# Performance work log

Hardware: AMD Instinct MI355X
Metric: run time of the kernel (lower is better)

Reference implementation:

```python
import jax, jax.numpy as jnp
import numpy as np

H = 16        # num_attention_heads
KV = 4        # num_key_value_heads
HD = 128      # head_dim = hidden_size // H
ROPE_THETA = 10000.0


def _rotate_half(x):
    x1, x2 = jnp.split(x, 2, axis=-1)
    return jnp.concatenate([-x2, x1], axis=-1)


def _rope_cos_sin(seq_len, dtype):
    # inv_freq: (HD//2,), full rotary (partial_rotary_factor=1.0), attention_scaling=1.0
    inv_freq = 1.0 / (ROPE_THETA ** (jnp.arange(0, HD, 2, dtype=jnp.float32) / HD))
    pos = jnp.arange(seq_len, dtype=jnp.float32)
    freqs = pos[:, None] * inv_freq[None, :]              # (S, HD//2)
    emb = jnp.concatenate([freqs, freqs], axis=-1)        # (S, HD)
    # expansion_axis=2 -> broadcast over heads: (1, S, 1, HD)
    return (jnp.cos(emb)[None, :, None, :].astype(dtype),
            jnp.sin(emb)[None, :, None, :].astype(dtype))


def setup_inputs() -> dict:
    key = jax.random.key(0)
    k1, k2, k3, k4, k5 = jax.random.split(key, 5)
    B, S, D = 2, 2048, 2048
    hidden_states = jax.random.normal(k1, (B, S, D), dtype=jnp.float32)
    # causal mask, True = attend
    causal = jnp.tril(jnp.ones((S, S), dtype=bool))
    attention_mask = jnp.broadcast_to(causal[None, None, :, :], (B, 1, S, S))
    scale = 0.02
    Wq = jax.random.normal(k2, (D, H * HD), dtype=jnp.float32) * scale
    Wk = jax.random.normal(k3, (D, KV * HD), dtype=jnp.float32) * scale
    Wv = jax.random.normal(k4, (D, KV * HD), dtype=jnp.float32) * scale
    Wo = jax.random.normal(k5, (H, HD, D), dtype=jnp.float32) * scale
    return {"hidden_states": hidden_states, "attention_mask": attention_mask,
            "Wq": Wq, "Wk": Wk, "Wv": Wv, "Wo": Wo}


def reference(hidden_states, attention_mask, Wq, Wk, Wv, Wo):
    B, S, D = hidden_states.shape
    q = (hidden_states @ Wq).reshape(B, S, H, HD)   # bquh
    k = (hidden_states @ Wk).reshape(B, S, KV, HD)
    v = (hidden_states @ Wv).reshape(B, S, KV, HD)

    cos, sin = _rope_cos_sin(S, q.dtype)
    q = q * cos + _rotate_half(q) * sin
    k = k * cos + _rotate_half(k) * sin

    # GQA: repeat kv heads to match query heads
    groups = H // KV
    k = jnp.repeat(k, groups, axis=2)               # (B, S, H, HD)
    v = jnp.repeat(v, groups, axis=2)

    inv_norm = 1.0 / np.sqrt(HD)
    scores = jnp.einsum('bquh,bkuh->buqk', q, k) * inv_norm   # (B, H, Sq, Sk)
    scores = scores.astype(jnp.float32)
    neg = jnp.asarray(-1e9, dtype=jnp.float32)
    scores = jnp.where(attention_mask, scores, neg)
    probs = jax.nn.softmax(scores, axis=-1).astype(q.dtype)
    attn = jnp.einsum('buqk,bkuh->bquh', probs, v)             # (B, S, H, HD)
    out = jnp.einsum('bquh,uhm->bqm', attn, Wo)                # (B, S, D)
    return out
```

## Files before the change

### kernel.cpp

```cpp
#include <hip/hip_runtime.h>
#include <math.h>

namespace {

constexpr int B   = 2;
constexpr int S   = 2048;
constexpr int D   = 2048;
constexpr int NH  = 16;
constexpr int NKV = 4;
constexpr int HD  = 128;
constexpr int GRP = NH / NKV;

typedef __attribute__((ext_vector_type(8))) short  short8;
typedef __attribute__((ext_vector_type(4))) float  f32x4;
typedef unsigned short u16;

__device__ inline u16 f2bf(float f) {
    unsigned u = __float_as_uint(f);
    u = (u + 0x7FFFu + ((u >> 16) & 1u)) >> 16;
    return (u16)u;
}
__device__ inline float bf2f(u16 h) {
    return __uint_as_float((unsigned)h << 16);
}

__device__ __forceinline__ void gload_lds16(const void* g, void* l) {
    __builtin_amdgcn_global_load_lds(
        (const __attribute__((address_space(1))) unsigned int*)g,
        (__attribute__((address_space(3))) unsigned int*)l, 16, 0, 0);
}

__global__ __launch_bounds__(256)
void split_cast_kernel(const float* __restrict__ X, u16* __restrict__ H,
                       u16* __restrict__ L, int n4)
{
    const int idx = blockIdx.x * 256 + threadIdx.x;
    if (idx >= n4) return;
    const float4 v = reinterpret_cast<const float4*>(X)[idx];
    ushort4 h, l;
    h.x = f2bf(v.x); l.x = f2bf(v.x - bf2f(h.x));
    h.y = f2bf(v.y); l.y = f2bf(v.y - bf2f(h.y));
    h.z = f2bf(v.z); l.z = f2bf(v.z - bf2f(h.z));
    h.w = f2bf(v.w); l.w = f2bf(v.w - bf2f(h.w));
    reinterpret_cast<ushort4*>(H)[idx] = h;
    reinterpret_cast<ushort4*>(L)[idx] = l;
}

__global__ __launch_bounds__(256)
void wcast_t_kernel(const float* __restrict__ W, u16* __restrict__ Th,
                    u16* __restrict__ Tl, int Nw, int n_off)
{
    __shared__ u16 th[64][68];
    __shared__ u16 tl[64][68];
    const int t  = threadIdx.x;
    const int n0 = blockIdx.x * 64;
    const int k0 = blockIdx.y * 64;

#pragma unroll
    for (int i = 0; i < 4; ++i) {
        const int kr = (t >> 4) + i * 16;
        const int nc = (t & 15) * 4;
        const float4 v = *reinterpret_cast<const float4*>(
            &W[(size_t)(k0 + kr) * Nw + n0 + nc]);
        const u16 hx = f2bf(v.x), hy = f2bf(v.y), hz = f2bf(v.z), hw = f2bf(v.w);
        th[kr][nc + 0] = hx; tl[kr][nc + 0] = f2bf(v.x - bf2f(hx));
        th[kr][nc + 1] = hy; tl[kr][nc + 1] = f2bf(v.y - bf2f(hy));
        th[kr][nc + 2] = hz; tl[kr][nc + 2] = f2bf(v.z - bf2f(hz));
        th[kr][nc + 3] = hw; tl[kr][nc + 3] = f2bf(v.w - bf2f(hw));
    }
    __syncthreads();
#pragma unroll
    for (int i = 0; i < 4; ++i) {
        const int nr = (t >> 4) + i * 16;
        const int kc = (t & 15) * 4;
        ushort4 oh, ol;
        oh.x = th[kc + 0][nr]; ol.x = tl[kc + 0][nr];
        oh.y = th[kc + 1][nr]; ol.y = tl[kc + 1][nr];
        oh.z = th[kc + 2][nr]; ol.z = tl[kc + 2][nr];
        oh.w = th[kc + 3][nr]; ol.w = tl[kc + 3][nr];
        const size_t o = (size_t)(n_off + n0 + nr) * 2048 + k0 + kc;
        *reinterpret_cast<ushort4*>(&Th[o]) = oh;
        *reinterpret_cast<ushort4*>(&Tl[o]) = ol;
    }
}

__global__ __launch_bounds__(256)
void hgemm_hilo_kernel(const u16* __restrict__ Ah, const u16* __restrict__ Al,
                       const u16* __restrict__ Bth, const u16* __restrict__ Btl,
                       float* __restrict__ C, int M, int N, int K)
{
    __shared__ alignas(16) u16 AsH[4096];
    __shared__ alignas(16) u16 AsL[4096];
    __shared__ alignas(16) u16 BsH[4096];
    __shared__ alignas(16) u16 BsL[4096];

    const int t  = threadIdx.x;
    const int w  = t >> 6;
    const int l  = t & 63;
    const int lc = l & 15;
    const int kg = l >> 4;
    const int wr = w >> 1, wc = w & 1;

    const int m0 = blockIdx.y * 128;
    const int n0 = blockIdx.x * 128;

    const int srow = l >> 2;
    const int sblk = l & 3;

    f32x4 acc[4][4];
#pragma unroll
    for (int i = 0; i < 4; ++i)
#pragma unroll
        for (int j = 0; j < 4; ++j) acc[i][j] = (f32x4){0.f, 0.f, 0.f, 0.f};

    for (int k0 = 0; k0 < K; k0 += 32) {
#pragma unroll
        for (int i = 0; i < 2; ++i) {
            const int c   = i * 4 + w;
            const int row = c * 16 + srow;
            const int swb = sblk ^ ((row >> 1) & 3);
            const size_t ga = (size_t)(m0 + row) * K + k0 + swb * 8;
            const size_t gb = (size_t)(n0 + row) * K + k0 + swb * 8;
            u16* ldst = (u16*)nullptr;
            (void)ldst;
            gload_lds16(Ah  + ga, AsH + c * 512);
            gload_lds16(Al  + ga, AsL + c * 512);
            gload_lds16(Bth + gb, BsH + c * 512);
            gload_lds16(Btl + gb, BsL + c * 512);
        }
        __syncthreads();

        short8 fah[4], fal[4], fbh[4], fbl[4];
#pragma unroll
        for (int i = 0; i < 4; ++i) {
            const int ra = wr * 64 + i * 16 + lc;
            const int oa = ra * 32 + ((kg ^ ((ra >> 1) & 3)) * 8);
            fah[i] = *reinterpret_cast<const short8*>(&AsH[oa]);
            fal[i] = *reinterpret_cast<const short8*>(&AsL[oa]);
            const int rb = wc * 64 + i * 16 + lc;
            const int ob = rb * 32 + ((kg ^ ((rb >> 1) & 3)) * 8);
            fbh[i] = *reinterpret_cast<const short8*>(&BsH[ob]);
            fbl[i] = *reinterpret_cast<const short8*>(&BsL[ob]);
        }
#pragma unroll
        for (int i = 0; i < 4; ++i)
#pragma unroll
            for (int j = 0; j < 4; ++j) {
                acc[i][j] = __builtin_amdgcn_mfma_f32_16x16x32_bf16(
                    fal[i], fbh[j], acc[i][j], 0, 0, 0);
                acc[i][j] = __builtin_amdgcn_mfma_f32_16x16x32_bf16(
                    fah[i], fbl[j], acc[i][j], 0, 0, 0);
                acc[i][j] = __builtin_amdgcn_mfma_f32_16x16x32_bf16(
                    fah[i], fbh[j], acc[i][j], 0, 0, 0);
            }
        __syncthreads();
    }

#pragma unroll
    for (int i = 0; i < 4; ++i)
#pragma unroll
        for (int j = 0; j < 4; ++j)
#pragma unroll
            for (int r = 0; r < 4; ++r) {
                const int m = m0 + wr * 64 + i * 16 + kg * 4 + r;
                const int n = n0 + wc * 64 + j * 16 + lc;
                C[(size_t)m * N + n] = acc[i][j][r];
            }
}

__global__ __launch_bounds__(256)
void rope_cast_kernel(const float* __restrict__ X, int stride, int col_off,
                      u16* __restrict__ Yh, u16* __restrict__ Yl,
                      int n_heads, int total_pairs, float scale)
{
    const int idx = blockIdx.x * 256 + threadIdx.x;
    if (idx >= total_pairs) return;
    const int i    = idx & 63;
    const int rest = idx >> 6;
    const int head = rest % n_heads;
    const int row  = rest / n_heads;
    const int s    = row & (S - 1);
    const int b    = row >> 11;

    const float inv = expf(-9.2103403719761836f * (float)i * (1.0f / 64.0f));
    float sn, cs;
    sincosf((float)s * inv, &sn, &cs);

    const float* src = X + (size_t)row * stride + col_off + head * HD + i;
    const float x1 = src[0], x2 = src[64];
    const float y1 = (x1 * cs - x2 * sn) * scale;
    const float y2 = (x2 * cs + x1 * sn) * scale;

    const u16 h1 = f2bf(y1), h2 = f2bf(y2);
    const size_t o = ((size_t)(b * n_heads + head) * S + s) * HD + i;
    Yh[o] = h1;  Yh[o + 64] = h2;
    Yl[o]      = f2bf(y1 - bf2f(h1));
    Yl[o + 64] = f2bf(y2 - bf2f(h2));
}

__global__ __launch_bounds__(256)
void vcast_kernel(const float* __restrict__ V, int stride, int col_off,
                  u16* __restrict__ Yh, u16* __restrict__ Yl)
{
    __shared__ u16 th[64][68];
    __shared__ u16 tl[64][68];
    const int t  = threadIdx.x;
    const int s0 = blockIdx.x * 64, dv0 = blockIdx.y * 64;
    const int b  = blockIdx.z >> 2, u = blockIdx.z & 3;

#pragma unroll
    for (int i = 0; i < 4; ++i) {
        const int sr = (t >> 4) + i * 16;
        const int dc = (t & 15) * 4;
        const float4 v = *reinterpret_cast<const float4*>(
            &V[(size_t)(b * S + s0 + sr) * stride + col_off + u * HD + dv0 + dc]);
        const u16 hx = f2bf(v.x), hy = f2bf(v.y), hz = f2bf(v.z), hw = f2bf(v.w);
        th[sr][dc + 0] = hx; tl[sr][dc + 0] = f2bf(v.x - bf2f(hx));
        th[sr][dc + 1] = hy; tl[sr][dc + 1] = f2bf(v.y - bf2f(hy));
        th[sr][dc + 2] = hz; tl[sr][dc + 2] = f2bf(v.z - bf2f(hz));
        th[sr][dc + 3] = hw; tl[sr][dc + 3] = f2bf(v.w - bf2f(hw));
    }
    __syncthreads();
#pragma unroll
    for (int i = 0; i < 4; ++i) {
        const int dr = (t >> 4) + i * 16;
        const int sc = (t & 15) * 4;
        ushort4 oh, ol;
        oh.x = th[sc + 0][dr]; ol.x = tl[sc + 0][dr];
        oh.y = th[sc + 1][dr]; ol.y = tl[sc + 1][dr];
        oh.z = th[sc + 2][dr]; ol.z = tl[sc + 2][dr];
        oh.w = th[sc + 3][dr]; ol.w = tl[sc + 3][dr];
        const size_t o = ((size_t)(b * NKV + u) * HD + dv0 + dr) * S + s0 + sc;
        *reinterpret_cast<ushort4*>(&Yh[o]) = oh;
        *reinterpret_cast<ushort4*>(&Yl[o]) = ol;
    }
}

constexpr int QTILE = 64, KT = 32;

__global__ __launch_bounds__(256)
void flash_mfma_kernel(const u16* __restrict__ Qh, const u16* __restrict__ Ql,
                       const u16* __restrict__ Kh, const u16* __restrict__ Kl,
                       const u16* __restrict__ Vh, const u16* __restrict__ Vl,
                       u16* __restrict__ Oh, u16* __restrict__ Ol)
{
    __shared__ alignas(16) u16 smem[23552];
    u16* KsH = smem;
    u16* KsL = smem + 4096;
    u16* VtH = smem + 8192;
    u16* VtL = smem + 13312;
    u16* PH  = smem + 18432;
    u16* PL  = smem + 20992;

    const int t  = threadIdx.x;
    const int w  = t >> 6;
    const int ln = t & 63;
    const int lg = ln >> 4;
    const int lc = ln & 15;

    const int qt = (int)gridDim.x - 1 - (int)blockIdx.x;
    const int q0 = qt * QTILE;
    const int bh = blockIdx.y;
    const int b  = bh / NH, h = bh % NH, u = h / GRP;

    const size_t qbase = (size_t)(b * NH + h) * S * HD;
    const size_t kbase = (size_t)(b * NKV + u) * S * HD;
    const size_t vbase = (size_t)(b * NKV + u) * HD * S;

    {
        u16* QsH = smem;
        u16* QsL = smem + 8192;
#pragma unroll
        for (int i = 0; i < 4; ++i) {
            const int r = (t >> 4) + i * 16;
            const int blk = t & 15;
            const size_t src = qbase + (size_t)(q0 + r) * HD + blk * 8;
            const int dst = r * 128 + ((blk ^ (r & 7)) * 8);
            *reinterpret_cast<short8*>(&QsH[dst]) =
                *reinterpret_cast<const short8*>(&Qh[src]);
            *reinterpret_cast<short8*>(&QsL[dst]) =
                *reinterpret_cast<const short8*>(&Ql[src]);
        }
        __syncthreads();
    }
    short8 qah[4], qal[4];
#pragma unroll
    for (int ks = 0; ks < 4; ++ks) {
        const int qr = w * 16 + lc;
        const int off = qr * 128 + (((ks * 4 + lg) ^ (qr & 7)) * 8);
        qah[ks] = *reinterpret_cast<const short8*>(&smem[off]);
        qal[ks] = *reinterpret_cast<const short8*>(&smem[8192 + off]);
    }
    __syncthreads();

    f32x4 o[8];
#pragma unroll
    for (int i = 0; i < 8; ++i) o[i] = (f32x4){0.f, 0.f, 0.f, 0.f};
    float m_run[4] = {-1e30f, -1e30f, -1e30f, -1e30f};
    float l_run[4] = {0.f, 0.f, 0.f, 0.f};

    u16* PwH = PH + w * 640;
    u16* PwL = PL + w * 640;
    const int qw0 = q0 + w * 16;
    const int nkt = q0 / KT + 2;

    for (int kt = 0; kt < nkt; ++kt) {
        const int k0 = kt * KT;
#pragma unroll
        for (int i = 0; i < 2; ++i) {
            const int r = (t >> 4) + i * 16;
            const int blk = t & 15;
            const size_t src = kbase + (size_t)(k0 + r) * HD + blk * 8;
            const int dst = r * 128 + ((blk ^ (r & 7)) * 8);
            *reinterpret_cast<short8*>(&KsH[dst]) =
                *reinterpret_cast<const short8*>(&Kh[src]);
            *reinterpret_cast<short8*>(&KsL[dst]) =
                *reinterpret_cast<const short8*>(&Kl[src]);
        }
#pragma unroll
        for (int i = 0; i < 2; ++i) {
            const int dv = (t >> 2) + i * 64;
            const int blk = t & 3;
            const size_t src = vbase + (size_t)dv * S + k0 + blk * 8;
            const int dst = dv * 40 + blk * 8;
            *reinterpret_cast<short8*>(&VtH[dst]) =
                *reinterpret_cast<const short8*>(&Vh[src]);
            *reinterpret_cast<short8*>(&VtL[dst]) =
                *reinterpret_cast<const short8*>(&Vl[src]);
        }
        __syncthreads();

        f32x4 a0 = {0.f, 0.f, 0.f, 0.f}, a1 = {0.f, 0.f, 0.f, 0.f};
#pragma unroll
        for (int ks = 0; ks < 4; ++ks) {
            const int r0 = lc, r1 = 16 + lc;
            const int o0b = r0 * 128 + (((ks * 4 + lg) ^ (r0 & 7)) * 8);
            const int o1b = r1 * 128 + (((ks * 4 + lg) ^ (r1 & 7)) * 8);
            const short8 kb0h = *reinterpret_cast<const short8*>(&KsH[o0b]);
            const short8 kb0l = *reinterpret_cast<const short8*>(&KsL[o0b]);
            const short8 kb1h = *reinterpret_cast<const short8*>(&KsH[o1b]);
            const short8 kb1l = *reinterpret_cast<const short8*>(&KsL[o1b]);
            a0 = __builtin_amdgcn_mfma_f32_16x16x32_bf16(qal[ks], kb0h, a0, 0, 0, 0);
            a0 = __builtin_amdgcn_mfma_f32_16x16x32_bf16(qah[ks], kb0l, a0, 0, 0, 0);
            a0 = __builtin_amdgcn_mfma_f32_16x16x32_bf16(qah[ks], kb0h, a0, 0, 0, 0);
            a1 = __builtin_amdgcn_mfma_f32_16x16x32_bf16(qal[ks], kb1h, a1, 0, 0, 0);
            a1 = __builtin_amdgcn_mfma_f32_16x16x32_bf16(qah[ks], kb1l, a1, 0, 0, 0);
            a1 = __builtin_amdgcn_mfma_f32_16x16x32_bf16(qah[ks], kb1h, a1, 0, 0, 0);
        }

        const bool need_mask = (k0 + KT - 1 > qw0);
#pragma unroll
        for (int r = 0; r < 4; ++r) {
            float s0 = a0[r], s1 = a1[r];
            const int qg = qw0 + lg * 4 + r;
            if (need_mask) {
                if (k0 + lc > qg)      s0 = -1e30f;
                if (k0 + 16 + lc > qg) s1 = -1e30f;
            }
            float mx = fmaxf(s0, s1);
            mx = fmaxf(mx, __shfl_xor(mx, 1, 64));
            mx = fmaxf(mx, __shfl_xor(mx, 2, 64));
            mx = fmaxf(mx, __shfl_xor(mx, 4, 64));
            mx = fmaxf(mx, __shfl_xor(mx, 8, 64));
            const float mn  = fmaxf(m_run[r], mx);
            const float rsc = __expf(m_run[r] - mn);
            const float p0  = __expf(s0 - mn);
            const float p1  = __expf(s1 - mn);
            float rs = p0 + p1;
            rs += __shfl_xor(rs, 1, 64);
            rs += __shfl_xor(rs, 2, 64);
            rs += __shfl_xor(rs, 4, 64);
            rs += __shfl_xor(rs, 8, 64);
            l_run[r] = l_run[r] * rsc + rs;
            m_run[r] = mn;
#pragma unroll
            for (int nt = 0; nt < 8; ++nt) o[nt][r] *= rsc;
            const u16 p0h = f2bf(p0);
            const u16 p1h = f2bf(p1);
            const int row = (lg * 4 + r) * 40;
            PwH[row + lc]      = p0h;
            PwH[row + 16 + lc] = p1h;
            PwL[row + lc]      = f2bf(p0 - bf2f(p0h));
            PwL[row + 16 + lc] = f2bf(p1 - bf2f(p1h));
        }
        asm volatile("s_waitcnt lgkmcnt(0)" ::: "memory");

        const short8 pah = *reinterpret_cast<const short8*>(&PwH[lc * 40 + lg * 8]);
        const short8 pal = *reinterpret_cast<const short8*>(&PwL[lc * 40 + lg * 8]);
#pragma unroll
        for (int nt = 0; nt < 8; ++nt) {
            const int dvo = (nt * 16 + lc) * 40 + lg * 8;
            const short8 vbh = *reinterpret_cast<const short8*>(&VtH[dvo]);
            const short8 vbl = *reinterpret_cast<const short8*>(&VtL[dvo]);
            o[nt] = __builtin_amdgcn_mfma_f32_16x16x32_bf16(pal, vbh, o[nt], 0, 0, 0);
            o[nt] = __builtin_amdgcn_mfma_f32_16x16x32_bf16(pah, vbl, o[nt], 0, 0, 0);
            o[nt] = __builtin_amdgcn_mfma_f32_16x16x32_bf16(pah, vbh, o[nt], 0, 0, 0);
        }
        __syncthreads();
    }

    float invl[4];
#pragma unroll
    for (int r = 0; r < 4; ++r) invl[r] = 1.f / l_run[r];
#pragma unroll
    for (int nt = 0; nt < 8; ++nt) {
#pragma unroll
        for (int r = 0; r < 4; ++r) {
            const float v = o[nt][r] * invl[r];
            const size_t off =
                (size_t)(b * S + qw0 + lg * 4 + r) * (NH * HD) + h * HD + nt * 16 + lc;
            const u16 hv = f2bf(v);
            Oh[off] = hv;
            Ol[off] = f2bf(v - bf2f(hv));
        }
    }
}

}

extern "C" void kernel_launch(void* const* d_in, const int* in_sizes, int n_in,
                              void* d_out, int out_size, void* d_ws, size_t ws_size,
                              hipStream_t stream)
{
    const float* hidden = (const float*)d_in[0];
    const float* Wq = (const float*)d_in[2];
    const float* Wk = (const float*)d_in[3];
    const float* Wv = (const float*)d_in[4];
    const float* Wo = (const float*)d_in[5];
    float* out = (float*)d_out;

    char* wsb = (char*)d_ws;
    u16*   hid_hi  = (u16*)(wsb);
    u16*   hid_lo  = (u16*)(wsb + 16777216);
    float* qkv_f   = (float*)(wsb + 33554432);
    u16*   k_hi    = (u16*)(wsb + 83886080);
    u16*   k_lo    = (u16*)(wsb + 88080384);
    u16*   v_hi    = (u16*)(wsb + 92274688);
    u16*   v_lo    = (u16*)(wsb + 96468992);
    u16*   wT_hi   = (u16*)(wsb + 100663296);
    u16*   wT_lo   = (u16*)(wsb + 113246208);
    u16* q_hi    = hid_hi;
    u16* q_lo    = hid_lo;
    u16* attn_hi = (u16*)(wsb + 33554432);
    u16* attn_lo = (u16*)(wsb + 50331648);
    u16* woT_hi  = wT_hi;
    u16* woT_lo  = wT_lo;

    const dim3 blk(256);

    split_cast_kernel<<<dim3(8192), blk, 0, stream>>>(hidden, hid_hi, hid_lo, 2097152);
    wcast_t_kernel<<<dim3(32, 32), blk, 0, stream>>>(Wq, wT_hi, wT_lo, 2048, 0);
    wcast_t_kernel<<<dim3(8, 32),  blk, 0, stream>>>(Wk, wT_hi, wT_lo, 512, 2048);
    wcast_t_kernel<<<dim3(8, 32),  blk, 0, stream>>>(Wv, wT_hi, wT_lo, 512, 2560);
    hgemm_hilo_kernel<<<dim3(24, 32), blk, 0, stream>>>(
        hid_hi, hid_lo, wT_hi, wT_lo, qkv_f, 4096, 3072, 2048);
    wcast_t_kernel<<<dim3(32, 32), blk, 0, stream>>>(Wo, woT_hi, woT_lo, 2048, 0);
    const int qpairs = 4096 * NH * 64;
    const int kpairs = 4096 * NKV * 64;
    rope_cast_kernel<<<dim3(qpairs / 256), blk, 0, stream>>>(
        qkv_f, 3072, 0, q_hi, q_lo, NH, qpairs, 0.08838834764831845f);
    rope_cast_kernel<<<dim3(kpairs / 256), blk, 0, stream>>>(
        qkv_f, 3072, 2048, k_hi, k_lo, NKV, kpairs, 1.0f);
    vcast_kernel<<<dim3(32, 2, 8), blk, 0, stream>>>(
        qkv_f, 3072, 2560, v_hi, v_lo);
    flash_mfma_kernel<<<dim3(S / QTILE, B * NH), blk, 0, stream>>>(
        q_hi, q_lo, k_hi, k_lo, v_hi, v_lo, attn_hi, attn_lo);
    hgemm_hilo_kernel<<<dim3(16, 32), blk, 0, stream>>>(
        attn_hi, attn_lo, woT_hi, woT_lo, out, 4096, 2048, 2048);
}
```

Before: 807.3 us.

## Load Q/K/V fragments directly from global, drop LDS staging and block syncs

The flash attention kernel now reads Q, K and V MFMA fragments straight from global memory into registers instead of staging them cooperatively in shared memory. Removing the staging also drops the per-tile __syncthreads, so each wave iterates independently and stops at its own causal limit (qw0/KT+1) instead of the block-wide limit. The MFMA blocks are wrapped in s_setprio to favour matrix issue. The cost is that the four waves, and sibling heads in a GQA group, now each fetch the same K/V data separately, which raises global and L2 traffic and register pressure.

```diff
diff --git a/kernel.cpp b/kernel.cpp
--- a/kernel.cpp
+++ b/kernel.cpp
@@ -121,8 +121,6 @@
             const int swb = sblk ^ ((row >> 1) & 3);
             const size_t ga = (size_t)(m0 + row) * K + k0 + swb * 8;
             const size_t gb = (size_t)(n0 + row) * K + k0 + swb * 8;
-            u16* ldst = (u16*)nullptr;
-            (void)ldst;
             gload_lds16(Ah  + ga, AsH + c * 512);
             gload_lds16(Al  + ga, AsL + c * 512);
             gload_lds16(Bth + gb, BsH + c * 512);
@@ -244,13 +242,8 @@
                        const u16* __restrict__ Vh, const u16* __restrict__ Vl,
                        u16* __restrict__ Oh, u16* __restrict__ Ol)
 {
-    __shared__ alignas(16) u16 smem[23552];
-    u16* KsH = smem;
-    u16* KsL = smem + 4096;
-    u16* VtH = smem + 8192;
-    u16* VtL = smem + 13312;
-    u16* PH  = smem + 18432;
-    u16* PL  = smem + 20992;
+    __shared__ alignas(16) u16 PHs[4 * 640];
+    __shared__ alignas(16) u16 PLs[4 * 640];
 
     const int t  = threadIdx.x;
     const int w  = t >> 6;
@@ -267,31 +260,17 @@
     const size_t kbase = (size_t)(b * NKV + u) * S * HD;
     const size_t vbase = (size_t)(b * NKV + u) * HD * S;
 
+    const int qw0 = q0 + w * 16;
+
+    short8 qah[4], qal[4];
     {
-        u16* QsH = smem;
-        u16* QsL = smem + 8192;
-#pragma unroll
-        for (int i = 0; i < 4; ++i) {
-            const int r = (t >> 4) + i * 16;
-            const int blk = t & 15;
-            const size_t src = qbase + (size_t)(q0 + r) * HD + blk * 8;
-            const int dst = r * 128 + ((blk ^ (r & 7)) * 8);
-            *reinterpret_cast<short8*>(&QsH[dst]) =
-                *reinterpret_cast<const short8*>(&Qh[src]);
-            *reinterpret_cast<short8*>(&QsL[dst]) =
-                *reinterpret_cast<const short8*>(&Ql[src]);
-        }
-        __syncthreads();
-    }
-    short8 qah[4], qal[4];
-#pragma unroll
-    for (int ks = 0; ks < 4; ++ks) {
-        const int qr = w * 16 + lc;
-        const int off = qr * 128 + (((ks * 4 + lg) ^ (qr & 7)) * 8);
-        qah[ks] = *reinterpret_cast<const short8*>(&smem[off]);
-        qal[ks] = *reinterpret_cast<const short8*>(&smem[8192 + off]);
-    }
-    __syncthreads();
+        const size_t qr = qbase + (size_t)(qw0 + lc) * HD + lg * 8;
+#pragma unroll
+        for (int ks = 0; ks < 4; ++ks) {
+            qah[ks] = *reinterpret_cast<const short8*>(&Qh[qr + ks * 32]);
+            qal[ks] = *reinterpret_cast<const short8*>(&Ql[qr + ks * 32]);
+        }
+    }
 
     f32x4 o[8];
 #pragma unroll
@@ -299,53 +278,46 @@
     float m_run[4] = {-1e30f, -1e30f, -1e30f, -1e30f};
     float l_run[4] = {0.f, 0.f, 0.f, 0.f};
 
-    u16* PwH = PH + w * 640;
-    u16* PwL = PL + w * 640;
-    const int qw0 = q0 + w * 16;
-    const int nkt = q0 / KT + 2;
+    u16* PwH = PHs + w * 640;
+    u16* PwL = PLs + w * 640;
+
+    const int nkt = qw0 / KT + 1;
 
     for (int kt = 0; kt < nkt; ++kt) {
         const int k0 = kt * KT;
-#pragma unroll
-        for (int i = 0; i < 2; ++i) {
-            const int r = (t >> 4) + i * 16;
-            const int blk = t & 15;
-            const size_t src = kbase + (size_t)(k0 + r) * HD + blk * 8;
-            const int dst = r * 128 + ((blk ^ (r & 7)) * 8);
-            *reinterpret_cast<short8*>(&KsH[dst]) =
-                *reinterpret_cast<const short8*>(&Kh[src]);
-            *reinterpret_cast<short8*>(&KsL[dst]) =
-                *reinterpret_cast<const short8*>(&Kl[src]);
-        }
-#pragma unroll
-        for (int i = 0; i < 2; ++i) {
-            const int dv = (t >> 2) + i * 64;
-            const int blk = t & 3;
-            const size_t src = vbase + (size_t)dv * S + k0 + blk * 8;
-            const int dst = dv * 40 + blk * 8;
-            *reinterpret_cast<short8*>(&VtH[dst]) =
-                *reinterpret_cast<const short8*>(&Vh[src]);
-            *reinterpret_cast<short8*>(&VtL[dst]) =
-                *reinterpret_cast<const short8*>(&Vl[src]);
-        }
-        __syncthreads();
+
+        short8 kb0h[4], kb0l[4], kb1h[4], kb1l[4];
+        {
+            const size_t kr0 = kbase + (size_t)(k0 + lc) * HD + lg * 8;
+            const size_t kr1 = kr0 + (size_t)16 * HD;
+#pragma unroll
+            for (int ks = 0; ks < 4; ++ks) {
+                kb0h[ks] = *reinterpret_cast<const short8*>(&Kh[kr0 + ks * 32]);
+                kb0l[ks] = *reinterpret_cast<const short8*>(&Kl[kr0 + ks * 32]);
+                kb1h[ks] = *reinterpret_cast<const short8*>(&Kh[kr1 + ks * 32]);
+                kb1l[ks] = *reinterpret_cast<const short8*>(&Kl[kr1 + ks * 32]);
+            }
+        }
 
         f32x4 a0 = {0.f, 0.f, 0.f, 0.f}, a1 = {0.f, 0.f, 0.f, 0.f};
+        __builtin_amdgcn_s_setprio(1);
 #pragma unroll
         for (int ks = 0; ks < 4; ++ks) {
-            const int r0 = lc, r1 = 16 + lc;
-            const int o0b = r0 * 128 + (((ks * 4 + lg) ^ (r0 & 7)) * 8);
-            const int o1b = r1 * 128 + (((ks * 4 + lg) ^ (r1 & 7)) * 8);
-            const short8 kb0h = *reinterpret_cast<const short8*>(&KsH[o0b]);
-            const short8 kb0l = *reinterpret_cast<const short8*>(&KsL[o0b]);
-            const short8 kb1h = *reinterpret_cast<const short8*>(&KsH[o1b]);
-            const short8 kb1l = *reinterpret_cast<const short8*>(&KsL[o1b]);
-            a0 = __builtin_amdgcn_mfma_f32_16x16x32_bf16(qal[ks], kb0h, a0, 0, 0, 0);
-            a0 = __builtin_amdgcn_mfma_f32_16x16x32_bf16(qah[ks], kb0l, a0, 0, 0, 0);
-            a0 = __builtin_amdgcn_mfma_f32_16x16x32_bf16(qah[ks], kb0h, a0, 0, 0, 0);
-            a1 = __builtin_amdgcn_mfma_f32_16x16x32_bf16(qal[ks], kb1h, a1, 0, 0, 0);
-            a1 = __builtin_amdgcn_mfma_f32_16x16x32_bf16(qah[ks], kb1l, a1, 0, 0, 0);
-            a1 = __builtin_amdgcn_mfma_f32_16x16x32_bf16(qah[ks], kb1h, a1, 0, 0, 0);
+            a0 = __builtin_amdgcn_mfma_f32_16x16x32_bf16(qal[ks], kb0h[ks], a0, 0, 0, 0);
+            a0 = __builtin_amdgcn_mfma_f32_16x16x32_bf16(qah[ks], kb0l[ks], a0, 0, 0, 0);
+            a0 = __builtin_amdgcn_mfma_f32_16x16x32_bf16(qah[ks], kb0h[ks], a0, 0, 0, 0);
+            a1 = __builtin_amdgcn_mfma_f32_16x16x32_bf16(qal[ks], kb1h[ks], a1, 0, 0, 0);
+            a1 = __builtin_amdgcn_mfma_f32_16x16x32_bf16(qah[ks], kb1l[ks], a1, 0, 0, 0);
+            a1 = __builtin_amdgcn_mfma_f32_16x16x32_bf16(qah[ks], kb1h[ks], a1, 0, 0, 0);
+        }
+        __builtin_amdgcn_s_setprio(0);
+
+        short8 vbh[8], vbl[8];
+#pragma unroll
+        for (int nt = 0; nt < 8; ++nt) {
+            const size_t vo = vbase + (size_t)(nt * 16 + lc) * S + k0 + lg * 8;
+            vbh[nt] = *reinterpret_cast<const short8*>(&Vh[vo]);
+            vbl[nt] = *reinterpret_cast<const short8*>(&Vl[vo]);
         }
 
         const bool need_mask = (k0 + KT - 1 > qw0);
@@ -387,16 +359,14 @@
 
         const short8 pah = *reinterpret_cast<const short8*>(&PwH[lc * 40 + lg * 8]);
         const short8 pal = *reinterpret_cast<const short8*>(&PwL[lc * 40 + lg * 8]);
+        __builtin_amdgcn_s_setprio(1);
 #pragma unroll
         for (int nt = 0; nt < 8; ++nt) {
-            const int dvo = (nt * 16 + lc) * 40 + lg * 8;
-            const short8 vbh = *reinterpret_cast<const short8*>(&VtH[dvo]);
-            const short8 vbl = *reinterpret_cast<const short8*>(&VtL[dvo]);
-            o[nt] = __builtin_amdgcn_mfma_f32_16x16x32_bf16(pal, vbh, o[nt], 0, 0, 0);
-            o[nt] = __builtin_amdgcn_mfma_f32_16x16x32_bf16(pah, vbl, o[nt], 0, 0, 0);
-            o[nt] = __builtin_amdgcn_mfma_f32_16x16x32_bf16(pah, vbh, o[nt], 0, 0, 0);
-        }
-        __syncthreads();
+            o[nt] = __builtin_amdgcn_mfma_f32_16x16x32_bf16(pal, vbh[nt], o[nt], 0, 0, 0);
+            o[nt] = __builtin_amdgcn_mfma_f32_16x16x32_bf16(pah, vbl[nt], o[nt], 0, 0, 0);
+            o[nt] = __builtin_amdgcn_mfma_f32_16x16x32_bf16(pah, vbh[nt], o[nt], 0, 0, 0);
+        }
+        __builtin_amdgcn_s_setprio(0);
     }
 
     float invl[4];
```

Result: slower. 1.329 ms (+64.7%).

## Prefetch next K/V tile into registers and add lazy softmax rescaling in attention

Applied to the files above, without the earlier changes.

The attention loop now loads the next K/V tile from global memory into registers while computing on the current tile in LDS, overlapping global latency with the MFMA work. Warps whose 16 query rows lie entirely above the current key tile skip that tile's compute. The online softmax rescales the output only when a row max grows by more than 8, checked wave-wide, and the per-row reductions are batched so shuffles interleave. s_setprio is raised around the MFMA blocks. The register staging adds VGPR pressure, which can reduce occupancy, and the lazy max leaves exponentials bounded by e^8 rather than 1.

```diff
diff --git a/kernel.cpp b/kernel.cpp
--- a/kernel.cpp
+++ b/kernel.cpp
@@ -121,8 +121,6 @@
             const int swb = sblk ^ ((row >> 1) & 3);
             const size_t ga = (size_t)(m0 + row) * K + k0 + swb * 8;
             const size_t gb = (size_t)(n0 + row) * K + k0 + swb * 8;
-            u16* ldst = (u16*)nullptr;
-            (void)ldst;
             gload_lds16(Ah  + ga, AsH + c * 512);
             gload_lds16(Al  + ga, AsL + c * 512);
             gload_lds16(Bth + gb, BsH + c * 512);
@@ -304,100 +302,150 @@
     const int qw0 = q0 + w * 16;
     const int nkt = q0 / KT + 2;
 
+    const int sr_k = t >> 4;
+    const int sb_k = t & 15;
+    const int sr_v = t >> 2;
+    const int sb_v = t & 3;
+    const int dKsw = (sb_k ^ (sr_k & 7)) * 8;
+    const int dK0  = sr_k * 128 + dKsw;
+    const int dK1  = (sr_k + 16) * 128 + dKsw;
+    const int dV0  = sr_v * 40 + sb_v * 8;
+    const int dV1  = (sr_v + 64) * 40 + sb_v * 8;
+
+    short8 stg[8];
+#define LOADTILE(K0)                                                          \
+    {                                                                         \
+        const size_t ksrc = kbase + (size_t)((K0) + sr_k) * HD + sb_k * 8;    \
+        stg[0] = *reinterpret_cast<const short8*>(&Kh[ksrc]);                 \
+        stg[1] = *reinterpret_cast<const short8*>(&Kh[ksrc + 16 * HD]);       \
+        stg[2] = *reinterpret_cast<const short8*>(&Kl[ksrc]);                 \
+        stg[3] = *reinterpret_cast<const short8*>(&Kl[ksrc + 16 * HD]);       \
+        const size_t vsrc = vbase + (size_t)sr_v * S + (K0) + sb_v * 8;       \
+        stg[4] = *reinterpret_cast<const short8*>(&Vh[vsrc]);                 \
+        stg[5] = *reinterpret_cast<const short8*>(&Vh[vsrc + (size_t)64 * S]);\
+        stg[6] = *reinterpret_cast<const short8*>(&Vl[vsrc]);                 \
+        stg[7] = *reinterpret_cast<const short8*>(&Vl[vsrc + (size_t)64 * S]);\
+    }
+
+    LOADTILE(0);
+
     for (int kt = 0; kt < nkt; ++kt) {
         const int k0 = kt * KT;
-#pragma unroll
-        for (int i = 0; i < 2; ++i) {
-            const int r = (t >> 4) + i * 16;
-            const int blk = t & 15;
-            const size_t src = kbase + (size_t)(k0 + r) * HD + blk * 8;
-            const int dst = r * 128 + ((blk ^ (r & 7)) * 8);
-            *reinterpret_cast<short8*>(&KsH[dst]) =
-                *reinterpret_cast<const short8*>(&Kh[src]);
-            *reinterpret_cast<short8*>(&KsL[dst]) =
-                *reinterpret_cast<const short8*>(&Kl[src]);
-        }
-#pragma unroll
-        for (int i = 0; i < 2; ++i) {
-            const int dv = (t >> 2) + i * 64;
-            const int blk = t & 3;
-            const size_t src = vbase + (size_t)dv * S + k0 + blk * 8;
-            const int dst = dv * 40 + blk * 8;
-            *reinterpret_cast<short8*>(&VtH[dst]) =
-                *reinterpret_cast<const short8*>(&Vh[src]);
-            *reinterpret_cast<short8*>(&VtL[dst]) =
-                *reinterpret_cast<const short8*>(&Vl[src]);
+        *reinterpret_cast<short8*>(&KsH[dK0]) = stg[0];
+        *reinterpret_cast<short8*>(&KsH[dK1]) = stg[1];
+        *reinterpret_cast<short8*>(&KsL[dK0]) = stg[2];
+        *reinterpret_cast<short8*>(&KsL[dK1]) = stg[3];
+        *reinterpret_cast<short8*>(&VtH[dV0]) = stg[4];
+        *reinterpret_cast<short8*>(&VtH[dV1]) = stg[5];
+        *reinterpret_cast<short8*>(&VtL[dV0]) = stg[6];
+        *reinterpret_cast<short8*>(&VtL[dV1]) = stg[7];
+        __syncthreads();
+
+        if (kt + 1 < nkt) LOADTILE(k0 + KT);
+
+        if (k0 <= qw0 + 15) {
+            f32x4 a0 = {0.f, 0.f, 0.f, 0.f}, a1 = {0.f, 0.f, 0.f, 0.f};
+            __builtin_amdgcn_s_setprio(1);
+#pragma unroll
+            for (int ks = 0; ks < 4; ++ks) {
+                const int r0 = lc, r1 = 16 + lc;
+                const int o0b = r0 * 128 + (((ks * 4 + lg) ^ (r0 & 7)) * 8);
+                const int o1b = r1 * 128 + (((ks * 4 + lg) ^ (r1 & 7)) * 8);
+                const short8 kb0h = *reinterpret_cast<const short8*>(&KsH[o0b]);
+                const short8 kb0l = *reinterpret_cast<const short8*>(&KsL[o0b]);
+                const short8 kb1h = *reinterpret_cast<const short8*>(&KsH[o1b]);
+                const short8 kb1l = *reinterpret_cast<const short8*>(&KsL[o1b]);
+                a0 = __builtin_amdgcn_mfma_f32_16x16x32_bf16(qal[ks], kb0h, a0, 0, 0, 0);
+                a0 = __builtin_amdgcn_mfma_f32_16x16x32_bf16(qah[ks], kb0l, a0, 0, 0, 0);
+                a0 = __builtin_amdgcn_mfma_f32_16x16x32_bf16(qah[ks], kb0h, a0, 0, 0, 0);
+                a1 = __builtin_amdgcn_mfma_f32_16x16x32_bf16(qal[ks], kb1h, a1, 0, 0, 0);
+                a1 = __builtin_amdgcn_mfma_f32_16x16x32_bf16(qah[ks], kb1l, a1, 0, 0, 0);
+                a1 = __builtin_amdgcn_mfma_f32_16x16x32_bf16(qah[ks], kb1h, a1, 0, 0, 0);
+            }
+            __builtin_amdgcn_s_setprio(0);
+
+            float s0v[4], s1v[4], mx[4];
+            const bool need_mask = (k0 + KT - 1 > qw0);
+#pragma unroll
+            for (int r = 0; r < 4; ++r) {
+                float s0 = a0[r], s1 = a1[r];
+                const int qg = qw0 + lg * 4 + r;
+                if (need_mask) {
+                    if (k0 + lc > qg)      s0 = -1e30f;
+                    if (k0 + 16 + lc > qg) s1 = -1e30f;
+                }
+                s0v[r] = s0; s1v[r] = s1;
+                mx[r] = fmaxf(s0, s1);
+            }
+#pragma unroll
+            for (int off = 1; off < 16; off <<= 1)
+#pragma unroll
+                for (int r = 0; r < 4; ++r)
+                    mx[r] = fmaxf(mx[r], __shfl_xor(mx[r], off, 64));
+
+            bool grow = false;
+#pragma unroll
+            for (int r = 0; r < 4; ++r) grow = grow || (mx[r] > m_run[r] + 8.0f);
+            const bool resc_needed = __any((int)grow);
+
+            float mn[4], rsc[4];
+#pragma unroll
+            for (int r = 0; r < 4; ++r) {
+                mn[r]  = resc_needed ? fmaxf(m_run[r], mx[r]) : m_run[r];
+                rsc[r] = resc_needed ? __expf(m_run[r] - mn[r]) : 1.0f;
+            }
+            float p0[4], p1[4], rs[4];
+#pragma unroll
+            for (int r = 0; r < 4; ++r) {
+                p0[r] = __expf(s0v[r] - mn[r]);
+                p1[r] = __expf(s1v[r] - mn[r]);
+                rs[r] = p0[r] + p1[r];
+            }
+#pragma unroll
+            for (int off = 1; off < 16; off <<= 1)
+#pragma unroll
+                for (int r = 0; r < 4; ++r)
+                    rs[r] += __shfl_xor(rs[r], off, 64);
+#pragma unroll
+            for (int r = 0; r < 4; ++r) {
+                l_run[r] = l_run[r] * rsc[r] + rs[r];
+                m_run[r] = mn[r];
+            }
+            if (resc_needed) {
+#pragma unroll
+                for (int nt = 0; nt < 8; ++nt)
+#pragma unroll
+                    for (int r = 0; r < 4; ++r) o[nt][r] *= rsc[r];
+            }
+#pragma unroll
+            for (int r = 0; r < 4; ++r) {
+                const u16 p0h = f2bf(p0[r]);
+                const u16 p1h = f2bf(p1[r]);
+                const int row = (lg * 4 + r) * 40;
+                PwH[row + lc]      = p0h;
+                PwH[row + 16 + lc] = p1h;
+                PwL[row + lc]      = f2bf(p0[r] - bf2f(p0h));
+                PwL[row + 16 + lc] = f2bf(p1[r] - bf2f(p1h));
+            }
+            asm volatile("s_waitcnt lgkmcnt(0)" ::: "memory");
+
+            const short8 pah = *reinterpret_cast<const short8*>(&PwH[lc * 40 + lg * 8]);
+            const short8 pal = *reinterpret_cast<const short8*>(&PwL[lc * 40 + lg * 8]);
+            __builtin_amdgcn_s_setprio(1);
+#pragma unroll
+            for (int nt = 0; nt < 8; ++nt) {
+                const int dvo = (nt * 16 + lc) * 40 + lg * 8;
+                const short8 vbh = *reinterpret_cast<const short8*>(&VtH[dvo]);
+                const short8 vbl = *reinterpret_cast<const short8*>(&VtL[dvo]);
+                o[nt] = __builtin_amdgcn_mfma_f32_16x16x32_bf16(pal, vbh, o[nt], 0, 0, 0);
+                o[nt] = __builtin_amdgcn_mfma_f32_16x16x32_bf16(pah, vbl, o[nt], 0, 0, 0);
+                o[nt] = __builtin_amdgcn_mfma_f32_16x16x32_bf16(pah, vbh, o[nt], 0, 0, 0);
+            }
+            __builtin_amdgcn_s_setprio(0);
         }
         __syncthreads();
-
-        f32x4 a0 = {0.f, 0.f, 0.f, 0.f}, a1 = {0.f, 0.f, 0.f, 0.f};
-#pragma unroll
-        for (int ks = 0; ks < 4; ++ks) {
-            const int r0 = lc, r1 = 16 + lc;
-            const int o0b = r0 * 128 + (((ks * 4 + lg) ^ (r0 & 7)) * 8);
-            const int o1b = r1 * 128 + (((ks * 4 + lg) ^ (r1 & 7)) * 8);
-            const short8 kb0h = *reinterpret_cast<const short8*>(&KsH[o0b]);
-            const short8 kb0l = *reinterpret_cast<const short8*>(&KsL[o0b]);
-            const short8 kb1h = *reinterpret_cast<const short8*>(&KsH[o1b]);
-            const short8 kb1l = *reinterpret_cast<const short8*>(&KsL[o1b]);
-            a0 = __builtin_amdgcn_mfma_f32_16x16x32_bf16(qal[ks], kb0h, a0, 0, 0, 0);
-            a0 = __builtin_amdgcn_mfma_f32_16x16x32_bf16(qah[ks], kb0l, a0, 0, 0, 0);
-            a0 = __builtin_amdgcn_mfma_f32_16x16x32_bf16(qah[ks], kb0h, a0, 0, 0, 0);
-            a1 = __builtin_amdgcn_mfma_f32_16x16x32_bf16(qal[ks], kb1h, a1, 0, 0, 0);
-            a1 = __builtin_amdgcn_mfma_f32_16x16x32_bf16(qah[ks], kb1l, a1, 0, 0, 0);
-            a1 = __builtin_amdgcn_mfma_f32_16x16x32_bf16(qah[ks], kb1h, a1, 0, 0, 0);
-        }
-
-        const bool need_mask = (k0 + KT - 1 > qw0);
-#pragma unroll
-        for (int r = 0; r < 4; ++r) {
-            float s0 = a0[r], s1 = a1[r];
-            const int qg = qw0 + lg * 4 + r;
-            if (need_mask) {
-                if (k0 + lc > qg)      s0 = -1e30f;
-                if (k0 + 16 + lc > qg) s1 = -1e30f;
-            }
-            float mx = fmaxf(s0, s1);
-            mx = fmaxf(mx, __shfl_xor(mx, 1, 64));
-            mx = fmaxf(mx, __shfl_xor(mx, 2, 64));
-            mx = fmaxf(mx, __shfl_xor(mx, 4, 64));
-            mx = fmaxf(mx, __shfl_xor(mx, 8, 64));
-            const float mn  = fmaxf(m_run[r], mx);
-            const float rsc = __expf(m_run[r] - mn);
-            const float p0  = __expf(s0 - mn);
-            const float p1  = __expf(s1 - mn);
-            float rs = p0 + p1;
-            rs += __shfl_xor(rs, 1, 64);
-            rs += __shfl_xor(rs, 2, 64);
-            rs += __shfl_xor(rs, 4, 64);
-            rs += __shfl_xor(rs, 8, 64);
-            l_run[r] = l_run[r] * rsc + rs;
-            m_run[r] = mn;
-#pragma unroll
-            for (int nt = 0; nt < 8; ++nt) o[nt][r] *= rsc;
-            const u16 p0h = f2bf(p0);
-            const u16 p1h = f2bf(p1);
-            const int row = (lg * 4 + r) * 40;
-            PwH[row + lc]      = p0h;
-            PwH[row + 16 + lc] = p1h;
-            PwL[row + lc]      = f2bf(p0 - bf2f(p0h));
-            PwL[row + 16 + lc] = f2bf(p1 - bf2f(p1h));
-        }
-        asm volatile("s_waitcnt lgkmcnt(0)" ::: "memory");
-
-        const short8 pah = *reinterpret_cast<const short8*>(&PwH[lc * 40 + lg * 8]);
-        const short8 pal = *reinterpret_cast<const short8*>(&PwL[lc * 40 + lg * 8]);
-#pragma unroll
-        for (int nt = 0; nt < 8; ++nt) {
-            const int dvo = (nt * 16 + lc) * 40 + lg * 8;
-            const short8 vbh = *reinterpret_cast<const short8*>(&VtH[dvo]);
-            const short8 vbl = *reinterpret_cast<const short8*>(&VtL[dvo]);
-            o[nt] = __builtin_amdgcn_mfma_f32_16x16x32_bf16(pal, vbh, o[nt], 0, 0, 0);
-            o[nt] = __builtin_amdgcn_mfma_f32_16x16x32_bf16(pah, vbl, o[nt], 0, 0, 0);
-            o[nt] = __builtin_amdgcn_mfma_f32_16x16x32_bf16(pah, vbh, o[nt], 0, 0, 0);
-        }
-        __syncthreads();
-    }
+    }
+#undef LOADTILE
 
     float invl[4];
 #pragma unroll
```

Measured after the change: 797.6 us. No clear change (-1.2%).
